# Kernel optimization log

Measured on AMD Instinct MI355X. Metric: run time of the kernel, lower is better.

The kernel has to match this reference:

```python
import jax, jax.numpy as jnp
from jax import lax
import numpy as np

INPUT_DIMS = 512
HIDDEN_DIMS = 1024
OUTPUT_DIMS = 512
BATCH = 64
T = 256


def setup_inputs() -> dict:
    key = jax.random.key(0)
    ks = jax.random.split(key, 9)
    s_ih = 1.0 / np.sqrt(HIDDEN_DIMS)
    inp = {
        "x": jax.random.normal(ks[0], (BATCH, INPUT_DIMS, T), dtype=jnp.float32),
        # LSTMCell params (PyTorch gate order: i, f, g, o)
        "W_ih": jax.random.uniform(ks[1], (4 * HIDDEN_DIMS, INPUT_DIMS), minval=-s_ih, maxval=s_ih, dtype=jnp.float32),
        "W_hh": jax.random.uniform(ks[2], (4 * HIDDEN_DIMS, HIDDEN_DIMS), minval=-s_ih, maxval=s_ih, dtype=jnp.float32),
        "b_ih": jax.random.uniform(ks[3], (4 * HIDDEN_DIMS,), minval=-s_ih, maxval=s_ih, dtype=jnp.float32),
        "b_hh": jax.random.uniform(ks[4], (4 * HIDDEN_DIMS,), minval=-s_ih, maxval=s_ih, dtype=jnp.float32),
        # Output linear
        "W_out": jax.random.uniform(ks[5], (OUTPUT_DIMS, HIDDEN_DIMS), minval=-s_ih, maxval=s_ih, dtype=jnp.float32),
        "b_out": jax.random.uniform(ks[6], (OUTPUT_DIMS,), minval=-s_ih, maxval=s_ih, dtype=jnp.float32),
        # Initial state (learned-ish constants in the original, sampled from randn)
        "h0": jax.random.normal(ks[7], (1, HIDDEN_DIMS), dtype=jnp.float32),
        "c0": jax.random.normal(ks[8], (1, HIDDEN_DIMS), dtype=jnp.float32),
    }
    return inp


def reference(x, W_ih, W_hh, b_ih, b_hh, W_out, b_out, h0, c0):
    B, I, Tlen = x.shape
    H = W_hh.shape[1]
    h = jnp.broadcast_to(h0, (B, H))
    c = jnp.broadcast_to(c0, (B, H))
    xs = jnp.transpose(x, (2, 0, 1))  # [T, B, I]
    # Precompute the input projection for all timesteps in one GEMM.
    x_proj = jnp.einsum("tbi,gi->tbg", xs, W_ih) + b_ih  # [T, B, 4H]

    def step(carry, xp):
        h, c = carry
        gates = xp + h @ W_hh.T + b_hh  # [B, 4H]
        i_g, f_g, g_g, o_g = jnp.split(gates, 4, axis=-1)
        i_g = jax.nn.sigmoid(i_g)
        f_g = jax.nn.sigmoid(f_g)
        g_g = jnp.tanh(g_g)
        o_g = jax.nn.sigmoid(o_g)
        c_new = f_g * c + i_g * g_g
        h_new = o_g * jnp.tanh(c_new)
        # NOTE: original applies the output head to the CELL state c, not h.
        p = jax.nn.softmax(c_new @ W_out.T + b_out, axis=1)  # [B, O]
        return (h_new, c_new), p

    _, ps = lax.scan(step, (h, c), x_proj)  # ps: [T, B, O]
    # torch.cat along dim 0 per timestep == stack then flatten first two dims.
    return ps.reshape(Tlen * B, -1)
```

## Files before the change

### kernel.cpp

```cpp
#include <hip/hip_runtime.h>


#define T_ 256

typedef __attribute__((ext_vector_type(8))) short bf16x8;
typedef __attribute__((ext_vector_type(4))) float floatx4;
typedef __attribute__((ext_vector_type(4))) int intx4;

__device__ __forceinline__ unsigned short f2bf(float f) {
  unsigned u = __builtin_bit_cast(unsigned, f);
  u += 0x7FFFu + ((u >> 16) & 1u);
  return (unsigned short)(u >> 16);
}

__device__ __forceinline__ float sigm(float x) { return 1.0f / (1.0f + __expf(-x)); }

__global__ void cvt_w(const float* __restrict__ w, unsigned short* __restrict__ o) {
  const size_t g = (size_t)blockIdx.x * 256 + threadIdx.x;
  const float* s = w + g * 8;
  bf16x8 v;
#pragma unroll
  for (int i = 0; i < 8; ++i) v[i] = (short)f2bf(s[i]);
  *(bf16x8*)(o + g * 8) = v;
}

__global__ void transpose_x(const float* __restrict__ x, unsigned short* __restrict__ xT) {
  __shared__ float tile[32][33];
  const int b = blockIdx.z, i0 = blockIdx.y * 32, t0 = blockIdx.x * 32;
  const int tx = threadIdx.x & 31, ty = threadIdx.x >> 5;
#pragma unroll
  for (int p = 0; p < 4; ++p) {
    const int i = ty + p * 8;
    tile[i][tx] = x[((size_t)b * 512 + i0 + i) * 256 + t0 + tx];
  }
  __syncthreads();
#pragma unroll
  for (int p = 0; p < 4; ++p) {
    const int t = ty + p * 8;
    xT[((size_t)(t0 + t) * 64 + b) * 512 + i0 + tx] = f2bf(tile[tx][t]);
  }
}

__global__ __launch_bounds__(512, 1) void lstm_rec(
    const float* __restrict__ Whh, const float* __restrict__ Wih,
    const float* __restrict__ bih, const float* __restrict__ bhh,
    const float* __restrict__ h0, const float* __restrict__ c0,
    const unsigned short* __restrict__ xT,
    unsigned short* __restrict__ hbuf,
    unsigned short* __restrict__ call,
    unsigned* __restrict__ flags)
{
  const int tid = threadIdx.x;
  const int lane = tid & 63;
  const int wv = tid >> 6;
  const int nh = wv & 1, kq = wv >> 1;
  const int mg = blockIdx.x & 3, ng = blockIdx.x >> 2;
  const int l15 = lane & 15, lq = lane >> 4;
  const int row = mg * 16 + l15;

  unsigned* grpflags = flags + mg * 64;
  unsigned* myflag   = grpflags + ng;

  __shared__ unsigned short hlds[16 * 1032];
  __shared__ float gpart[4][16][66];

  bf16x8 bfrag[2][12];
#pragma unroll
  for (int nt = 0; nt < 2; ++nt) {
    const int ncol = (2 * nh + nt) * 1024 + ng * 16 + l15;
#pragma unroll
    for (int ks = 0; ks < 12; ++ks) {
      const int kg = kq * 384 + ks * 32 + lq * 8;
      const float* s = (kg < 1024) ? (Whh + (size_t)ncol * 1024 + kg)
                                   : (Wih + (size_t)ncol * 512 + (kg - 1024));
      bf16x8 v;
#pragma unroll
      for (int i = 0; i < 8; ++i) v[i] = (short)f2bf(s[i]);
      bfrag[nt][ks] = v;
    }
  }

  const int m_loc = tid >> 4, j = tid & 15;
  const int row_g = mg * 16 + m_loc;
  const int unit = ng * 16 + j;
  float c_reg = 0.f, bs0 = 0.f, bs1 = 0.f, bs2 = 0.f, bs3 = 0.f;
  if (tid < 256) {
    c_reg = c0[unit];
    bs0 = bih[unit] + bhh[unit];
    bs1 = bih[1024 + unit] + bhh[1024 + unit];
    bs2 = bih[2048 + unit] + bhh[2048 + unit];
    bs3 = bih[3072 + unit] + bhh[3072 + unit];
    unsigned short* hp = hbuf + 65536 + row_g * 1024 + unit;
    const unsigned hv = f2bf(h0[unit]);
    asm volatile("global_store_short %0, %1, off sc0 sc1"
                 :: "v"(hp), "v"(hv) : "memory");
    asm volatile("s_waitcnt vmcnt(0)" ::: "memory");
  }
  __syncthreads();
  if (tid == 0)
    __hip_atomic_store(myflag, 1u, __ATOMIC_RELAXED, __HIP_MEMORY_SCOPE_SYSTEM);

  for (int t = 0; t < T_; ++t) {
    const unsigned short* bx = xT + ((size_t)t * 64 + row) * 512;
    floatx4 zero = {0.f, 0.f, 0.f, 0.f};
    floatx4 acc0 = zero, acc1 = zero;

#pragma unroll
    for (int ks = 0; ks < 12; ++ks) {
      const int kg = kq * 384 + ks * 32 + lq * 8;
      if (kg >= 1024) {
        const bf16x8 af = *(const bf16x8*)(bx + (kg - 1024));
        acc0 = __builtin_amdgcn_mfma_f32_16x16x32_bf16(af, bfrag[0][ks], acc0, 0, 0, 0);
        acc1 = __builtin_amdgcn_mfma_f32_16x16x32_bf16(af, bfrag[1][ks], acc1, 0, 0, 0);
      }
    }

    if (wv == 0) {
      const unsigned tgt = (unsigned)(t + 1);
      while (!__all(__hip_atomic_load(grpflags + lane, __ATOMIC_RELAXED,
                                      __HIP_MEMORY_SCOPE_SYSTEM) >= tgt)) {}
    }
    __syncthreads();

    {
      const unsigned short* hprev = hbuf + ((t + 1) & 1) * 65536;
      const unsigned short* gsrc = hprev + (size_t)(mg * 16) * 1024 + (size_t)tid * 8;
      intx4 a0, a1, a2, a3;
      asm volatile(
          "global_load_dwordx4 %0, %4, off sc0 sc1\n\t"
          "global_load_dwordx4 %1, %5, off sc0 sc1\n\t"
          "global_load_dwordx4 %2, %6, off sc0 sc1\n\t"
          "global_load_dwordx4 %3, %7, off sc0 sc1\n\t"
          "s_waitcnt vmcnt(0)"
          : "=v"(a0), "=v"(a1), "=v"(a2), "=v"(a3)
          : "v"(gsrc), "v"(gsrc + 4096), "v"(gsrc + 8192), "v"(gsrc + 12288)
          : "memory");
      intx4 av[4] = {a0, a1, a2, a3};
#pragma unroll
      for (int p = 0; p < 4; ++p) {
        const int e = tid + p * 512;
        const int r = e >> 7, col = (e & 127) * 8;
        *(intx4*)(hlds + r * 1032 + col) = av[p];
      }
    }
    __syncthreads();

#pragma unroll
    for (int ks = 0; ks < 12; ++ks) {
      const int kg = kq * 384 + ks * 32 + lq * 8;
      if (kg < 1024) {
        const bf16x8 af = *(const bf16x8*)(hlds + l15 * 1032 + kg);
        acc0 = __builtin_amdgcn_mfma_f32_16x16x32_bf16(af, bfrag[0][ks], acc0, 0, 0, 0);
        acc1 = __builtin_amdgcn_mfma_f32_16x16x32_bf16(af, bfrag[1][ks], acc1, 0, 0, 0);
      }
    }

#pragma unroll
    for (int r = 0; r < 4; ++r) {
      gpart[kq][lq * 4 + r][(2 * nh) * 16 + l15]     = acc0[r];
      gpart[kq][lq * 4 + r][(2 * nh + 1) * 16 + l15] = acc1[r];
    }
    __syncthreads();

    if (tid < 256) {
      float gi = bs0, gf = bs1, gg = bs2, go = bs3;
#pragma unroll
      for (int q = 0; q < 4; ++q) {
        gi += gpart[q][m_loc][j];
        gf += gpart[q][m_loc][16 + j];
        gg += gpart[q][m_loc][32 + j];
        go += gpart[q][m_loc][48 + j];
      }
      const float iv = sigm(gi), fv = sigm(gf), gv = tanhf(gg), ov = sigm(go);
      c_reg = fv * c_reg + iv * gv;
      const float hv = ov * tanhf(c_reg);
      call[((size_t)t * 64 + row_g) * 1024 + unit] = f2bf(c_reg);
      unsigned short* hp = hbuf + (t & 1) * 65536 + row_g * 1024 + unit;
      const unsigned hb = f2bf(hv);
      asm volatile("global_store_short %0, %1, off sc0 sc1"
                   :: "v"(hp), "v"(hb) : "memory");
      asm volatile("s_waitcnt vmcnt(0)" ::: "memory");
    }
    __syncthreads();
    if (tid == 0)
      __hip_atomic_store(myflag, (unsigned)(t + 2), __ATOMIC_RELAXED,
                         __HIP_MEMORY_SCOPE_SYSTEM);
  }
}

__global__ __launch_bounds__(256, 1) void lstm_head(
    const unsigned short* __restrict__ call,
    const unsigned short* __restrict__ wout,
    const float* __restrict__ bout,
    float* __restrict__ out)
{
  const int tb = blockIdx.x;
  const int lane = threadIdx.x & 63;
  const int wv = threadIdx.x >> 6;
  const int l15 = lane & 15, lq = lane >> 4;

  __shared__ float sred[2][4][64];

  floatx4 zero = {0.f, 0.f, 0.f, 0.f};
  floatx4 acc[4][8];
#pragma unroll
  for (int mt = 0; mt < 4; ++mt)
#pragma unroll
    for (int nt = 0; nt < 8; ++nt) acc[mt][nt] = zero;

  const unsigned short* abase = call + ((size_t)tb * 64 + l15) * 1024 + lq * 8;
  const unsigned short* bbase = wout + ((size_t)(wv * 128 + l15)) * 1024 + lq * 8;

#pragma unroll 2
  for (int ks = 0; ks < 32; ++ks) {
    bf16x8 a[4];
#pragma unroll
    for (int mt = 0; mt < 4; ++mt)
      a[mt] = *(const bf16x8*)(abase + (size_t)mt * 16 * 1024 + ks * 32);
#pragma unroll
    for (int nt = 0; nt < 8; ++nt) {
      const bf16x8 b = *(const bf16x8*)(bbase + (size_t)nt * 16 * 1024 + ks * 32);
#pragma unroll
      for (int mt = 0; mt < 4; ++mt)
        acc[mt][nt] = __builtin_amdgcn_mfma_f32_16x16x32_bf16(a[mt], b, acc[mt][nt], 0, 0, 0);
    }
  }

#pragma unroll
  for (int nt = 0; nt < 8; ++nt) {
    const float bo = bout[wv * 128 + nt * 16 + l15];
#pragma unroll
    for (int mt = 0; mt < 4; ++mt)
#pragma unroll
      for (int r = 0; r < 4; ++r) acc[mt][nt][r] += bo;
  }

  float rmax[4][4];
#pragma unroll
  for (int mt = 0; mt < 4; ++mt)
#pragma unroll
    for (int r = 0; r < 4; ++r) {
      float m = acc[mt][0][r];
#pragma unroll
      for (int nt = 1; nt < 8; ++nt) m = fmaxf(m, acc[mt][nt][r]);
      m = fmaxf(m, __shfl_xor(m, 1, 64));
      m = fmaxf(m, __shfl_xor(m, 2, 64));
      m = fmaxf(m, __shfl_xor(m, 4, 64));
      m = fmaxf(m, __shfl_xor(m, 8, 64));
      rmax[mt][r] = m;
    }
  if (l15 == 0) {
#pragma unroll
    for (int mt = 0; mt < 4; ++mt)
#pragma unroll
      for (int r = 0; r < 4; ++r) sred[0][wv][mt * 16 + lq * 4 + r] = rmax[mt][r];
  }
  __syncthreads();
  float gmax[4][4], rsum[4][4];
#pragma unroll
  for (int mt = 0; mt < 4; ++mt)
#pragma unroll
    for (int r = 0; r < 4; ++r) {
      const int rw = mt * 16 + lq * 4 + r;
      gmax[mt][r] = fmaxf(fmaxf(sred[0][0][rw], sred[0][1][rw]),
                          fmaxf(sred[0][2][rw], sred[0][3][rw]));
      rsum[mt][r] = 0.f;
    }
#pragma unroll
  for (int mt = 0; mt < 4; ++mt)
#pragma unroll
    for (int nt = 0; nt < 8; ++nt)
#pragma unroll
      for (int r = 0; r < 4; ++r) {
        const float e = __expf(acc[mt][nt][r] - gmax[mt][r]);
        acc[mt][nt][r] = e;
        rsum[mt][r] += e;
      }
#pragma unroll
  for (int mt = 0; mt < 4; ++mt)
#pragma unroll
    for (int r = 0; r < 4; ++r) {
      float s = rsum[mt][r];
      s += __shfl_xor(s, 1, 64);
      s += __shfl_xor(s, 2, 64);
      s += __shfl_xor(s, 4, 64);
      s += __shfl_xor(s, 8, 64);
      rsum[mt][r] = s;
    }
  if (l15 == 0) {
#pragma unroll
    for (int mt = 0; mt < 4; ++mt)
#pragma unroll
      for (int r = 0; r < 4; ++r) sred[1][wv][mt * 16 + lq * 4 + r] = rsum[mt][r];
  }
  __syncthreads();
#pragma unroll
  for (int mt = 0; mt < 4; ++mt)
#pragma unroll
    for (int r = 0; r < 4; ++r) {
      const int rw = mt * 16 + lq * 4 + r;
      const float inv = 1.0f / (sred[1][0][rw] + sred[1][1][rw] +
                                sred[1][2][rw] + sred[1][3][rw]);
      float* orow = out + ((size_t)tb * 64 + rw) * 512 + wv * 128 + l15;
#pragma unroll
      for (int nt = 0; nt < 8; ++nt) orow[nt * 16] = acc[mt][nt][r] * inv;
    }
}

extern "C" void kernel_launch(void* const* d_in, const int* in_sizes, int n_in,
                              void* d_out, int out_size, void* d_ws, size_t ws_size,
                              hipStream_t stream) {
  const float* x    = (const float*)d_in[0];
  const float* Wih  = (const float*)d_in[1];
  const float* Whh  = (const float*)d_in[2];
  const float* bih  = (const float*)d_in[3];
  const float* bhh  = (const float*)d_in[4];
  const float* Wout = (const float*)d_in[5];
  const float* bout = (const float*)d_in[6];
  const float* h0   = (const float*)d_in[7];
  const float* c0   = (const float*)d_in[8];
  float* out = (float*)d_out;

  char* ws = (char*)d_ws;
  unsigned* flags       = (unsigned*)(ws + 0);
  unsigned short* hbuf  = (unsigned short*)(ws + 4096);
  unsigned short* woutb = (unsigned short*)(ws + 266240);
  unsigned short* xT    = (unsigned short*)(ws + 1314816);
  unsigned short* call  = (unsigned short*)(ws + 18092032);

  hipMemsetAsync(flags, 0, 1024, stream);
  cvt_w<<<256, 256, 0, stream>>>(Wout, woutb);
  transpose_x<<<dim3(8, 16, 64), 256, 0, stream>>>(x, xT);
  lstm_rec<<<256, 512, 0, stream>>>(Whh, Wih, bih, bhh, h0, c0, xT, hbuf, call, flags);
  lstm_head<<<256, 256, 0, stream>>>(call, woutb, bout, out);
}
```

Before: 1.489 ms.

## Replace per-block flag barrier with parity-tagged hidden-state polling

Removes the global flag array and per-step flag spin-wait, and drops the store waitcnt and block barrier after each step. Each stored bf16 h value now carries a parity tag in bit 14 (the second-highest exponent bit), and consumers poll the h buffer directly until every loaded value has the expected tag, then mask the tag off. h0 is loaded straight into LDS at t=0, and the buffer is memset to 0xFF beforehand. This cuts a synchronization round trip per timestep. The tag relies on bit 14 being zero for the bf16 magnitudes that occur, which holds only while |h| stays below 2 (true for tanh-bounded h), and on a 2-step tag period over double buffering to tell stale data from fresh.

Result: faster. 1.314 ms (-11.7%).

```diff
diff --git a/kernel.cpp b/kernel.cpp
--- a/kernel.cpp
+++ b/kernel.cpp
@@ -47,8 +47,7 @@
     const float* __restrict__ h0, const float* __restrict__ c0,
     const unsigned short* __restrict__ xT,
     unsigned short* __restrict__ hbuf,
-    unsigned short* __restrict__ call,
-    unsigned* __restrict__ flags)
+    unsigned short* __restrict__ call)
 {
   const int tid = threadIdx.x;
   const int lane = tid & 63;
@@ -57,9 +56,6 @@
   const int mg = blockIdx.x & 3, ng = blockIdx.x >> 2;
   const int l15 = lane & 15, lq = lane >> 4;
   const int row = mg * 16 + l15;
-
-  unsigned* grpflags = flags + mg * 64;
-  unsigned* myflag   = grpflags + ng;
 
   __shared__ unsigned short hlds[16 * 1032];
   __shared__ float gpart[4][16][66];
@@ -90,15 +86,7 @@
     bs1 = bih[1024 + unit] + bhh[1024 + unit];
     bs2 = bih[2048 + unit] + bhh[2048 + unit];
     bs3 = bih[3072 + unit] + bhh[3072 + unit];
-    unsigned short* hp = hbuf + 65536 + row_g * 1024 + unit;
-    const unsigned hv = f2bf(h0[unit]);
-    asm volatile("global_store_short %0, %1, off sc0 sc1"
-                 :: "v"(hp), "v"(hv) : "memory");
-    asm volatile("s_waitcnt vmcnt(0)" ::: "memory");
-  }
-  __syncthreads();
-  if (tid == 0)
-    __hip_atomic_store(myflag, 1u, __ATOMIC_RELAXED, __HIP_MEMORY_SCOPE_SYSTEM);
+  }
 
   for (int t = 0; t < T_; ++t) {
     const unsigned short* bx = xT + ((size_t)t * 64 + row) * 512;
@@ -115,32 +103,51 @@
       }
     }
 
-    if (wv == 0) {
-      const unsigned tgt = (unsigned)(t + 1);
-      while (!__all(__hip_atomic_load(grpflags + lane, __ATOMIC_RELAXED,
-                                      __HIP_MEMORY_SCOPE_SYSTEM) >= tgt)) {}
-    }
-    __syncthreads();
-
-    {
-      const unsigned short* hprev = hbuf + ((t + 1) & 1) * 65536;
-      const unsigned short* gsrc = hprev + (size_t)(mg * 16) * 1024 + (size_t)tid * 8;
-      intx4 a0, a1, a2, a3;
-      asm volatile(
-          "global_load_dwordx4 %0, %4, off sc0 sc1\n\t"
-          "global_load_dwordx4 %1, %5, off sc0 sc1\n\t"
-          "global_load_dwordx4 %2, %6, off sc0 sc1\n\t"
-          "global_load_dwordx4 %3, %7, off sc0 sc1\n\t"
-          "s_waitcnt vmcnt(0)"
-          : "=v"(a0), "=v"(a1), "=v"(a2), "=v"(a3)
-          : "v"(gsrc), "v"(gsrc + 4096), "v"(gsrc + 8192), "v"(gsrc + 12288)
-          : "memory");
-      intx4 av[4] = {a0, a1, a2, a3};
+    if (t == 0) {
 #pragma unroll
       for (int p = 0; p < 4; ++p) {
         const int e = tid + p * 512;
         const int r = e >> 7, col = (e & 127) * 8;
-        *(intx4*)(hlds + r * 1032 + col) = av[p];
+        const float* s = h0 + col;
+        bf16x8 v;
+#pragma unroll
+        for (int i = 0; i < 8; ++i) v[i] = (short)f2bf(s[i]);
+        *(bf16x8*)(hlds + r * 1032 + col) = v;
+      }
+    } else {
+      const unsigned short* hprev = hbuf + ((t + 1) & 1) * 65536;
+      const unsigned short* gsrc = hprev + (size_t)(mg * 16) * 1024 + (size_t)tid * 8;
+      const unsigned tagpat = (((t - 1) >> 1) & 1) ? 0x40004000u : 0u;
+      intx4 a0, a1, a2, a3;
+      while (true) {
+        asm volatile(
+            "global_load_dwordx4 %0, %4, off sc0 sc1\n\t"
+            "global_load_dwordx4 %1, %5, off sc0 sc1\n\t"
+            "global_load_dwordx4 %2, %6, off sc0 sc1\n\t"
+            "global_load_dwordx4 %3, %7, off sc0 sc1\n\t"
+            "s_waitcnt vmcnt(0)"
+            : "=v"(a0), "=v"(a1), "=v"(a2), "=v"(a3)
+            : "v"(gsrc), "v"(gsrc + 4096), "v"(gsrc + 8192), "v"(gsrc + 12288)
+            : "memory");
+        unsigned bad = 0;
+#pragma unroll
+        for (int d = 0; d < 4; ++d) {
+          bad |= ((unsigned)a0[d] ^ tagpat) & 0x40004000u;
+          bad |= ((unsigned)a1[d] ^ tagpat) & 0x40004000u;
+          bad |= ((unsigned)a2[d] ^ tagpat) & 0x40004000u;
+          bad |= ((unsigned)a3[d] ^ tagpat) & 0x40004000u;
+        }
+        if (!bad) break;
+      }
+      intx4 av[4] = {a0, a1, a2, a3};
+#pragma unroll
+      for (int p = 0; p < 4; ++p) {
+        intx4 v = av[p];
+#pragma unroll
+        for (int d = 0; d < 4; ++d) v[d] &= (int)0xBFFFBFFFu;
+        const int e = tid + p * 512;
+        const int r = e >> 7, col = (e & 127) * 8;
+        *(intx4*)(hlds + r * 1032 + col) = v;
       }
     }
     __syncthreads();
@@ -176,15 +183,10 @@
       const float hv = ov * tanhf(c_reg);
       call[((size_t)t * 64 + row_g) * 1024 + unit] = f2bf(c_reg);
       unsigned short* hp = hbuf + (t & 1) * 65536 + row_g * 1024 + unit;
-      const unsigned hb = f2bf(hv);
+      const unsigned hb = (unsigned)f2bf(hv) | ((unsigned)((t >> 1) & 1) << 14);
       asm volatile("global_store_short %0, %1, off sc0 sc1"
                    :: "v"(hp), "v"(hb) : "memory");
-      asm volatile("s_waitcnt vmcnt(0)" ::: "memory");
-    }
-    __syncthreads();
-    if (tid == 0)
-      __hip_atomic_store(myflag, (unsigned)(t + 2), __ATOMIC_RELAXED,
-                         __HIP_MEMORY_SCOPE_SYSTEM);
+    }
   }
 }
 
@@ -322,15 +324,14 @@
   float* out = (float*)d_out;
 
   char* ws = (char*)d_ws;
-  unsigned* flags       = (unsigned*)(ws + 0);
   unsigned short* hbuf  = (unsigned short*)(ws + 4096);
   unsigned short* woutb = (unsigned short*)(ws + 266240);
   unsigned short* xT    = (unsigned short*)(ws + 1314816);
   unsigned short* call  = (unsigned short*)(ws + 18092032);
 
-  hipMemsetAsync(flags, 0, 1024, stream);
+  hipMemsetAsync(hbuf, 0xFF, 262144, stream);
   cvt_w<<<256, 256, 0, stream>>>(Wout, woutb);
   transpose_x<<<dim3(8, 16, 64), 256, 0, stream>>>(x, xT);
-  lstm_rec<<<256, 512, 0, stream>>>(Whh, Wih, bih, bhh, h0, c0, xT, hbuf, call, flags);
+  lstm_rec<<<256, 512, 0, stream>>>(Whh, Wih, bih, bhh, h0, c0, xT, hbuf, call);
   lstm_head<<<256, 256, 0, stream>>>(call, woutb, bout, out);
 }
```
